# Optimization experiments

Hardware: AMD Instinct MI355X
Metric: run time of the kernel (lower is better)

## Reference

```python
import jax, jax.numpy as jnp
import numpy as np

D_MODEL, N_HEADS = 768, 12
D_K = D_MODEL // N_HEADS
NEG = -1e9


def setup_inputs() -> dict:
    key = jax.random.key(0)
    ks = jax.random.split(key, 12)
    B, S, D = 2, 4096, D_MODEL
    s = 1.0 / np.sqrt(D)
    inp = {
        'query': jax.random.normal(ks[0], (B, S, D), jnp.float32),
        'key': jax.random.normal(ks[1], (B, S, D), jnp.float32),
        'value': jax.random.normal(ks[2], (B, S, D), jnp.float32),
        'mask': jnp.ones((B, S), jnp.int32),
        'Wq': jax.random.normal(ks[3], (D, D), jnp.float32) * s,
        'bq': jnp.zeros((D,), jnp.float32),
        'Wk': jax.random.normal(ks[4], (D, D), jnp.float32) * s,
        'bk': jnp.zeros((D,), jnp.float32),
        'Wv': jax.random.normal(ks[5], (D, D), jnp.float32) * s,
        'bv': jnp.zeros((D,), jnp.float32),
        'Wo': jax.random.normal(ks[6], (D, D), jnp.float32) * s,
        'bo': jnp.zeros((D,), jnp.float32),
    }
    return inp


def reference(query, key, value, mask, Wq, bq, Wk, bk, Wv, bv, Wo, bo):
    B, Sq, D = query.shape
    Sk = key.shape[1]
    # torch Linear: x @ W.T + b; weights stored [out, in]
    def proj(x, W, b, S):
        return (x @ W.T + b).reshape(B, S, N_HEADS, D_K).transpose(0, 2, 1, 3)
    Q = proj(query, Wq, bq, Sq)   # [B,H,Sq,Dk]
    K = proj(key, Wk, bk, Sk)
    V = proj(value, Wv, bv, Sk)
    scores = jnp.einsum('bhqd,bhkd->bhqk', Q, K) / jnp.sqrt(jnp.float32(D_K))
    # padding mask on keys: [B,1,1,Sk]
    scores = jnp.where(mask[:, None, None, :] == 0, NEG, scores)
    # causal mask (triu, diagonal=1)
    causal = jnp.triu(jnp.ones((Sq, Sk), bool), k=1)
    scores = jnp.where(causal[None, None], NEG, scores)
    attn = jax.nn.softmax(scores, axis=-1)
    out = jnp.einsum('bhqk,bhkd->bhqd', attn, V)
    out = out.transpose(0, 2, 1, 3).reshape(B, Sq, D)
    return out @ Wo.T + bo
```

## Files before the change

kernel.cpp:

```cpp
#include <hip/hip_runtime.h>
#include <hip/hip_bf16.h>

#define D_MODEL 768
#define N_HEADS 12
#define D_K     64
#define NEG_INF (-1e9f)
#define SCALE_Q 0.1803368801111154f
#define W_ELEMS (D_MODEL * D_MODEL)
#define PS_PAD  72
#define RED_PAD 36

typedef __attribute__((ext_vector_type(8))) short          bf16x8;
typedef __attribute__((ext_vector_type(4))) float          floatx4;
typedef __attribute__((ext_vector_type(4))) unsigned short ushortx4;
typedef __attribute__((ext_vector_type(2))) unsigned int   uintx2;

static __device__ __forceinline__ unsigned short f2bf(float f) {
    unsigned u = __builtin_bit_cast(unsigned, f);
    u += 0x7FFFu + ((u >> 16) & 1u);
    return (unsigned short)(u >> 16);
}

static __device__ __forceinline__ void gload_lds16(const void* g, void* l) {
    __builtin_amdgcn_global_load_lds(
        (const __attribute__((address_space(1))) void*)g,
        (__attribute__((address_space(3))) void*)l, 16, 0, 0);
}

__global__ __launch_bounds__(256) void convert_w4(
    const float* __restrict__ W0, const float* __restrict__ W1,
    const float* __restrict__ W2, const float* __restrict__ W3,
    unsigned short* __restrict__ out)
{
    const float* src[4] = {W0, W1, W2, W3};
    const float* W = src[blockIdx.y];
    unsigned short* o = out + (size_t)blockIdx.y * W_ELEMS;
    const int i = (blockIdx.x * 256 + threadIdx.x) * 4;
    float4 v = *(const float4*)(W + i);
    ushortx4 h = { f2bf(v.x), f2bf(v.y), f2bf(v.z), f2bf(v.w) };
    *(ushortx4*)(o + i) = h;
}

__global__ __launch_bounds__(256) void convert_a3(
    const float* __restrict__ A0, const float* __restrict__ A1,
    const float* __restrict__ A2,
    unsigned short* __restrict__ O0, unsigned short* __restrict__ O1,
    unsigned short* __restrict__ O2)
{
    const int z = blockIdx.y;
    const float* A = (z == 0) ? A0 : (z == 1) ? A1 : A2;
    unsigned short* O = (z == 0) ? O0 : (z == 1) ? O1 : O2;
    const int i = (blockIdx.x * 256 + threadIdx.x) * 4;
    float4 v = *(const float4*)(A + i);
    ushortx4 h = { f2bf(v.x), f2bf(v.y), f2bf(v.z), f2bf(v.w) };
    *(ushortx4*)(O + i) = h;
}

template <bool QKV>
__global__ __launch_bounds__(256) void gemm128(
    const unsigned short* __restrict__ A0, const unsigned short* __restrict__ A1,
    const unsigned short* __restrict__ A2,
    const unsigned short* __restrict__ W0, const unsigned short* __restrict__ W1,
    const unsigned short* __restrict__ W2,
    const float* __restrict__ b0, const float* __restrict__ b1,
    const float* __restrict__ b2,
    void* __restrict__ C0, void* __restrict__ C1, void* __restrict__ C2,
    int S)
{
    __shared__ __align__(16) unsigned short As[128 * 32];
    __shared__ __align__(16) unsigned short Bs[128 * 32];

    const int z = QKV ? blockIdx.z : 0;
    const unsigned short* A = (z == 0) ? A0 : (z == 1) ? A1 : A2;
    const unsigned short* W = (z == 0) ? W0 : (z == 1) ? W1 : W2;
    const float* bias       = (z == 0) ? b0 : (z == 1) ? b1 : b2;
    void* C                 = (z == 0) ? C0 : (z == 1) ? C1 : C2;
    const float scale = (QKV && z == 0) ? SCALE_Q : 1.0f;
    const int mode = QKV ? ((z == 2) ? 3 : 1) : 0;

    const int tid  = threadIdx.x;
    const int wave = tid >> 6;
    const int lane = tid & 63;
    const int quad = lane >> 4;
    const int l16  = lane & 15;
    const int m0 = blockIdx.x * 128;
    const int n0 = blockIdx.y * 128;
    const int wm = (wave & 1) * 64;
    const int wn = (wave >> 1) * 64;
    const int sr = lane >> 2;
    const int sc = (lane & 3) << 3;

    const floatx4 zero4 = {0.f, 0.f, 0.f, 0.f};
    floatx4 acc[4][4];
    #pragma unroll
    for (int i = 0; i < 4; ++i)
        #pragma unroll
        for (int j = 0; j < 4; ++j) acc[i][j] = zero4;

    for (int k0 = 0; k0 < D_MODEL; k0 += 32) {
        #pragma unroll
        for (int c = 0; c < 2; ++c) {
            const int row = wave * 32 + c * 16;
            gload_lds16(A + (size_t)(m0 + row + sr) * D_MODEL + k0 + sc,
                        As + row * 32);
            gload_lds16(W + (size_t)(n0 + row + sr) * D_MODEL + k0 + sc,
                        Bs + row * 32);
        }
        __syncthreads();

        bf16x8 af[4], bfr[4];
        #pragma unroll
        for (int i = 0; i < 4; ++i)
            af[i] = *(const bf16x8*)(As + (wm + i * 16 + l16) * 32 + quad * 8);
        #pragma unroll
        for (int j = 0; j < 4; ++j)
            bfr[j] = *(const bf16x8*)(Bs + (wn + j * 16 + l16) * 32 + quad * 8);
        #pragma unroll
        for (int i = 0; i < 4; ++i)
            #pragma unroll
            for (int j = 0; j < 4; ++j)
                acc[i][j] = __builtin_amdgcn_mfma_f32_16x16x32_bf16(
                    bfr[j], af[i], acc[i][j], 0, 0, 0);
        __syncthreads();
    }

    #pragma unroll
    for (int i = 0; i < 4; ++i) {
        const int m = m0 + wm + i * 16 + l16;
        #pragma unroll
        for (int j = 0; j < 4; ++j) {
            const int nb = n0 + wn + j * 16 + quad * 4;
            const float4 bv = *(const float4*)(bias + nb);
            float v0 = (acc[i][j][0] + bv.x) * scale;
            float v1 = (acc[i][j][1] + bv.y) * scale;
            float v2 = (acc[i][j][2] + bv.z) * scale;
            float v3 = (acc[i][j][3] + bv.w) * scale;
            if (mode == 0) {
                float4 o = {v0, v1, v2, v3};
                *(float4*)((float*)C + (size_t)m * D_MODEL + nb) = o;
            } else if (mode == 1) {
                ushortx4 o = {f2bf(v0), f2bf(v1), f2bf(v2), f2bf(v3)};
                *(ushortx4*)((unsigned short*)C + (size_t)m * D_MODEL + nb) = o;
            } else {
                const int bb = m / S, s = m - bb * S;
                const int hh = nb >> 6, d = nb & 63;
                unsigned short* base = (unsigned short*)C +
                    ((size_t)(bb * N_HEADS + hh) * D_K + d) * S + s;
                base[0]             = f2bf(v0);
                base[(size_t)S]     = f2bf(v1);
                base[(size_t)S * 2] = f2bf(v2);
                base[(size_t)S * 3] = f2bf(v3);
            }
        }
    }
}

union FlashSmem {
    struct {
        unsigned short KsF[16 * 512];
        unsigned short VtsF[16 * 512];
    } kv;
    struct {
        float red[2][64 * RED_PAD];
        float redl[2][32];
    } ep;
};

__global__ __launch_bounds__(256, 3) void flash_attn(
    const unsigned short* __restrict__ Qp,
    const unsigned short* __restrict__ Kp,
    const unsigned short* __restrict__ VpT,
    const int* __restrict__ mask,
    unsigned short* __restrict__ O,
    int S)
{
    __shared__ __align__(16) FlashSmem sm;
    __shared__ __align__(16) unsigned short Ps[4][32 * PS_PAD];
    __shared__ __align__(16) float mskf[128];

    const int L  = blockIdx.x;
    const int bh = L % 24;
    const int p  = L / 24;
    const int h  = bh % 12;
    const int b  = bh / 12;
    const int nqt = S >> 6;
    const int tid  = threadIdx.x;
    const int wave = tid >> 6;
    const int qw   = wave & 1;
    const int kw   = wave >> 1;
    const int lane = tid & 63;
    const int quad = lane >> 4;
    const int l16  = lane & 15;
    const int ksl  = kw * 64;

    const unsigned short* Kbase = Kp  + (size_t)(b * S) * D_MODEL + h * D_K;
    const unsigned short* Vbase = VpT + (size_t)(b * N_HEADS + h) * D_K * S;
    unsigned short* Psw = Ps[wave];

    const floatx4 zero4 = {0.f, 0.f, 0.f, 0.f};
    const short one_bf = (short)0x3F80;
    const bf16x8 ones = {one_bf, one_bf, one_bf, one_bf,
                         one_bf, one_bf, one_bf, one_bf};

    #pragma unroll
    for (int sel = 0; sel < 2; ++sel) {
        const int qt = sel ? (nqt - 1 - p) : p;
        const int q0 = qt * 64;
        const int qs = q0 + qw * 32;

        bf16x8 qf[2][2];
        #pragma unroll
        for (int qg = 0; qg < 2; ++qg) {
            const size_t rowQ = (size_t)(b * S + qs + qg * 16 + l16) * D_MODEL + h * D_K;
            qf[qg][0] = *(const bf16x8*)(Qp + rowQ + quad * 8);
            qf[qg][1] = *(const bf16x8*)(Qp + rowQ + 32 + quad * 8);
        }

        floatx4 accO[2][4];
        floatx4 accL[2];
        #pragma unroll
        for (int qg = 0; qg < 2; ++qg) {
            accL[qg] = zero4;
            #pragma unroll
            for (int dt = 0; dt < 4; ++dt) accO[qg][dt] = zero4;
        }

        const int ni = (qt >> 1) + 1;
        for (int kt = 0; kt < ni; ++kt) {
            const int k0 = kt * 128;
            #pragma unroll
            for (int c = 0; c < 4; ++c) {
                const int kg = wave * 2 + (c >> 1);
                const int kh = c & 1;
                gload_lds16(Kbase + (size_t)(k0 + kg * 16 + l16) * D_MODEL + kh * 32 + quad * 8,
                            sm.kv.KsF + (kg * 2 + kh) * 512);
                const int dt = wave;
                const int kq = c;
                gload_lds16(Vbase + (size_t)(dt * 16 + l16) * S + k0 + kq * 32 + quad * 8,
                            sm.kv.VtsF + (dt * 4 + kq) * 512);
            }
            if (tid < 128)
                mskf[tid] = (mask[b * S + k0 + tid] == 0) ? NEG_INF : 0.f;
            __syncthreads();

            const int kb = k0 + ksl;
            if (kb <= q0 + 63) {
                const bool diag = (kb + 63 > qs);

                #pragma unroll
                for (int nt = 0; nt < 4; ++nt) {
                    const floatx4 minit = *(const floatx4*)(mskf + ksl + nt * 16 + quad * 4);
                    const int kgf = (kw * 4 + nt) * 2;
                    const bf16x8 kf0 = *(const bf16x8*)(sm.kv.KsF + kgf * 512 + lane * 8);
                    const bf16x8 kf1 = *(const bf16x8*)(sm.kv.KsF + (kgf + 1) * 512 + lane * 8);
                    #pragma unroll
                    for (int qg = 0; qg < 2; ++qg) {
                        floatx4 c = minit;
                        c = __builtin_amdgcn_mfma_f32_16x16x32_bf16(kf0, qf[qg][0], c, 0, 0, 0);
                        c = __builtin_amdgcn_mfma_f32_16x16x32_bf16(kf1, qf[qg][1], c, 0, 0, 0);
                        if (diag) {
                            const int kk = kb + nt * 16 + quad * 4;
                            const int qq = qs + qg * 16 + l16;
                            #pragma unroll
                            for (int r = 0; r < 4; ++r)
                                if (kk + r > qq) c[r] = NEG_INF;
                        }
                        const float e0 = __builtin_exp2f(c[0]);
                        const float e1 = __builtin_exp2f(c[1]);
                        const float e2 = __builtin_exp2f(c[2]);
                        const float e3 = __builtin_exp2f(c[3]);
                        uintx2 pk;
                        pk[0] = __builtin_amdgcn_perm(__builtin_bit_cast(unsigned, e1),
                                                      __builtin_bit_cast(unsigned, e0), 0x07060302u);
                        pk[1] = __builtin_amdgcn_perm(__builtin_bit_cast(unsigned, e3),
                                                      __builtin_bit_cast(unsigned, e2), 0x07060302u);
                        *(uintx2*)(Psw + (qg * 16 + l16) * PS_PAD + nt * 16 + quad * 4) = pk;
                    }
                }

                #pragma unroll
                for (int kh = 0; kh < 2; ++kh) {
                    bf16x8 pf[2];
                    #pragma unroll
                    for (int qg = 0; qg < 2; ++qg)
                        pf[qg] = *(const bf16x8*)(Psw + (qg * 16 + l16) * PS_PAD + kh * 32 + quad * 8);
                    #pragma unroll
                    for (int dt = 0; dt < 4; ++dt) {
                        const bf16x8 vf = *(const bf16x8*)(
                            sm.kv.VtsF + (dt * 4 + kw * 2 + kh) * 512 + lane * 8);
                        #pragma unroll
                        for (int qg = 0; qg < 2; ++qg)
                            accO[qg][dt] = __builtin_amdgcn_mfma_f32_16x16x32_bf16(
                                pf[qg], vf, accO[qg][dt], 0, 0, 0);
                    }
                    #pragma unroll
                    for (int qg = 0; qg < 2; ++qg)
                        accL[qg] = __builtin_amdgcn_mfma_f32_16x16x32_bf16(
                            pf[qg], ones, accL[qg], 0, 0, 0);
                }
            }
            __syncthreads();
        }

        if (kw == 1) {
            float* rb = sm.ep.red[qw];
            #pragma unroll
            for (int qg = 0; qg < 2; ++qg) {
                #pragma unroll
                for (int dt = 0; dt < 4; ++dt)
                    *(floatx4*)(rb + (dt * 16 + l16) * RED_PAD + qg * 16 + quad * 4) = accO[qg][dt];
                if (l16 == 0)
                    *(floatx4*)(sm.ep.redl[qw] + qg * 16 + quad * 4) = accL[qg];
            }
        }
        __syncthreads();
        if (kw == 0) {
            const float* rb = sm.ep.red[qw];
            #pragma unroll
            for (int qg = 0; qg < 2; ++qg) {
                accL[qg] += *(const floatx4*)(sm.ep.redl[qw] + qg * 16 + quad * 4);
                #pragma unroll
                for (int dt = 0; dt < 4; ++dt)
                    accO[qg][dt] += *(const floatx4*)(rb + (dt * 16 + l16) * RED_PAD + qg * 16 + quad * 4);
                #pragma unroll
                for (int r = 0; r < 4; ++r) {
                    const float inv = 1.f / accL[qg][r];
                    const int gq = qs + qg * 16 + quad * 4 + r;
                    unsigned short* ob = O + (size_t)(b * S + gq) * D_MODEL + h * D_K;
                    #pragma unroll
                    for (int dt = 0; dt < 4; ++dt)
                        ob[dt * 16 + l16] = f2bf(accO[qg][dt][r] * inv);
                }
            }
        }
        __syncthreads();
    }
}

extern "C" void kernel_launch(void* const* d_in, const int* in_sizes, int n_in,
                              void* d_out, int out_size, void* d_ws, size_t ws_size,
                              hipStream_t stream) {
    const float* query = (const float*)d_in[0];
    const float* key   = (const float*)d_in[1];
    const float* value = (const float*)d_in[2];
    const int*   mask  = (const int*)d_in[3];
    const float* Wq = (const float*)d_in[4];
    const float* bq = (const float*)d_in[5];
    const float* Wk = (const float*)d_in[6];
    const float* bk = (const float*)d_in[7];
    const float* Wv = (const float*)d_in[8];
    const float* bv = (const float*)d_in[9];
    const float* Wo = (const float*)d_in[10];
    const float* bo = (const float*)d_in[11];

    const int B  = 2;
    const int BS = in_sizes[3];
    const int S  = BS / B;
    const int M  = BS;

    unsigned short* Qp  = (unsigned short*)d_ws;
    unsigned short* Kp  = Qp  + (size_t)M * D_MODEL;
    unsigned short* VpT = Kp  + (size_t)M * D_MODEL;
    unsigned short* Obf = VpT + (size_t)M * D_MODEL;
    unsigned short* Wbf = Obf + (size_t)M * D_MODEL;
    unsigned short* Wqb = Wbf;
    unsigned short* Wkb = Wbf + (size_t)W_ELEMS;
    unsigned short* Wvb = Wbf + (size_t)W_ELEMS * 2;
    unsigned short* Wob = Wbf + (size_t)W_ELEMS * 3;
    unsigned short* ka = (unsigned short*)d_out;
    unsigned short* va = ka + (size_t)M * D_MODEL;

    dim3 blk(256);
    convert_w4<<<dim3(W_ELEMS / 1024, 4), blk, 0, stream>>>(Wq, Wk, Wv, Wo, Wbf);
    convert_a3<<<dim3((M * D_MODEL) / 1024, 3), blk, 0, stream>>>(
        query, key, value, Obf, ka, va);

    gemm128<true><<<dim3(M / 128, D_MODEL / 128, 3), blk, 0, stream>>>(
        Obf, ka, va, Wqb, Wkb, Wvb, bq, bk, bv, Qp, Kp, VpT, S);

    flash_attn<<<768, blk, 0, stream>>>(Qp, Kp, VpT, mask, Obf, S);

    gemm128<false><<<dim3(M / 128, D_MODEL / 128, 1), blk, 0, stream>>>(
        Obf, Obf, Obf, Wob, Wob, Wob, bo, bo, bo,
        d_out, d_out, d_out, S);
}
```

Before: 320.8 us.

## Shrink attention tiles to one query tile per block and retile output GEMM

The attention kernel changes from paired query tiles per block (768 blocks, 128-key steps) to one 64-query tile per block (1536 blocks), launched heaviest-first, with 64-key steps and the P buffer moved into the shared-memory union. It skips the fully masked diagonal sub-block and raises the occupancy target to 5 blocks per CU. The output projection now uses a templated GEMM with 64-row tiles, doubling its block count. The aim is better load balance and occupancy in exchange for more loop iterations, more barriers, and less K/V reuse per block.

New measurement: 352.3 us. 1.1x slower.

```diff
diff --git a/kernel.cpp b/kernel.cpp
--- a/kernel.cpp
+++ b/kernel.cpp
@@ -7,7 +7,7 @@
 #define NEG_INF (-1e9f)
 #define SCALE_Q 0.1803368801111154f
 #define W_ELEMS (D_MODEL * D_MODEL)
-#define PS_PAD  72
+#define PS_PAD  40
 #define RED_PAD 36
 
 typedef __attribute__((ext_vector_type(8))) short          bf16x8;
@@ -56,8 +56,8 @@
     *(ushortx4*)(O + i) = h;
 }
 
-template <bool QKV>
-__global__ __launch_bounds__(256) void gemm128(
+template <int TM, bool QKV>
+__global__ __launch_bounds__(256) void gemm_bt(
     const unsigned short* __restrict__ A0, const unsigned short* __restrict__ A1,
     const unsigned short* __restrict__ A2,
     const unsigned short* __restrict__ W0, const unsigned short* __restrict__ W1,
@@ -67,7 +67,8 @@
     void* __restrict__ C0, void* __restrict__ C1, void* __restrict__ C2,
     int S)
 {
-    __shared__ __align__(16) unsigned short As[128 * 32];
+    constexpr int NI = TM / 32;
+    __shared__ __align__(16) unsigned short As[TM * 32];
     __shared__ __align__(16) unsigned short Bs[128 * 32];
 
     const int z = QKV ? blockIdx.z : 0;
@@ -83,40 +84,44 @@
     const int lane = tid & 63;
     const int quad = lane >> 4;
     const int l16  = lane & 15;
-    const int m0 = blockIdx.x * 128;
+    const int m0 = blockIdx.x * TM;
     const int n0 = blockIdx.y * 128;
-    const int wm = (wave & 1) * 64;
+    const int wm = (wave & 1) * (TM / 2);
     const int wn = (wave >> 1) * 64;
     const int sr = lane >> 2;
     const int sc = (lane & 3) << 3;
 
     const floatx4 zero4 = {0.f, 0.f, 0.f, 0.f};
-    floatx4 acc[4][4];
+    floatx4 acc[NI][4];
     #pragma unroll
-    for (int i = 0; i < 4; ++i)
+    for (int i = 0; i < NI; ++i)
         #pragma unroll
         for (int j = 0; j < 4; ++j) acc[i][j] = zero4;
 
     for (int k0 = 0; k0 < D_MODEL; k0 += 32) {
+        #pragma unroll
+        for (int c = 0; c < TM / 64; ++c) {
+            const int row = wave * (TM / 4) + c * 16;
+            gload_lds16(A + (size_t)(m0 + row + sr) * D_MODEL + k0 + sc,
+                        As + row * 32);
+        }
         #pragma unroll
         for (int c = 0; c < 2; ++c) {
             const int row = wave * 32 + c * 16;
-            gload_lds16(A + (size_t)(m0 + row + sr) * D_MODEL + k0 + sc,
-                        As + row * 32);
             gload_lds16(W + (size_t)(n0 + row + sr) * D_MODEL + k0 + sc,
                         Bs + row * 32);
         }
         __syncthreads();
 
-        bf16x8 af[4], bfr[4];
-        #pragma unroll
-        for (int i = 0; i < 4; ++i)
+        bf16x8 af[NI], bfr[4];
+        #pragma unroll
+        for (int i = 0; i < NI; ++i)
             af[i] = *(const bf16x8*)(As + (wm + i * 16 + l16) * 32 + quad * 8);
         #pragma unroll
         for (int j = 0; j < 4; ++j)
             bfr[j] = *(const bf16x8*)(Bs + (wn + j * 16 + l16) * 32 + quad * 8);
         #pragma unroll
-        for (int i = 0; i < 4; ++i)
+        for (int i = 0; i < NI; ++i)
             #pragma unroll
             for (int j = 0; j < 4; ++j)
                 acc[i][j] = __builtin_amdgcn_mfma_f32_16x16x32_bf16(
@@ -125,7 +130,7 @@
     }
 
     #pragma unroll
-    for (int i = 0; i < 4; ++i) {
+    for (int i = 0; i < NI; ++i) {
         const int m = m0 + wm + i * 16 + l16;
         #pragma unroll
         for (int j = 0; j < 4; ++j) {
@@ -157,8 +162,9 @@
 
 union FlashSmem {
     struct {
-        unsigned short KsF[16 * 512];
-        unsigned short VtsF[16 * 512];
+        unsigned short KsF[8 * 512];
+        unsigned short VtsF[8 * 512];
+        unsigned short Ps[4][32 * PS_PAD];
     } kv;
     struct {
         float red[2][64 * RED_PAD];
@@ -166,7 +172,7 @@
     } ep;
 };
 
-__global__ __launch_bounds__(256, 3) void flash_attn(
+__global__ __launch_bounds__(256, 5) void flash_attn(
     const unsigned short* __restrict__ Qp,
     const unsigned short* __restrict__ Kp,
     const unsigned short* __restrict__ VpT,
@@ -175,15 +181,14 @@
     int S)
 {
     __shared__ __align__(16) FlashSmem sm;
-    __shared__ __align__(16) unsigned short Ps[4][32 * PS_PAD];
-    __shared__ __align__(16) float mskf[128];
+    __shared__ __align__(16) float mskf[64];
 
     const int L  = blockIdx.x;
     const int bh = L % 24;
-    const int p  = L / 24;
+    const int nqt = S >> 6;
+    const int qt = (nqt - 1) - (L / 24);
     const int h  = bh % 12;
     const int b  = bh / 12;
-    const int nqt = S >> 6;
     const int tid  = threadIdx.x;
     const int wave = tid >> 6;
     const int qw   = wave & 1;
@@ -191,149 +196,134 @@
     const int lane = tid & 63;
     const int quad = lane >> 4;
     const int l16  = lane & 15;
-    const int ksl  = kw * 64;
+
+    const int q0 = qt * 64;
+    const int qs = q0 + qw * 32;
 
     const unsigned short* Kbase = Kp  + (size_t)(b * S) * D_MODEL + h * D_K;
     const unsigned short* Vbase = VpT + (size_t)(b * N_HEADS + h) * D_K * S;
-    unsigned short* Psw = Ps[wave];
 
     const floatx4 zero4 = {0.f, 0.f, 0.f, 0.f};
     const short one_bf = (short)0x3F80;
     const bf16x8 ones = {one_bf, one_bf, one_bf, one_bf,
                          one_bf, one_bf, one_bf, one_bf};
 
+    bf16x8 qf[2][2];
     #pragma unroll
-    for (int sel = 0; sel < 2; ++sel) {
-        const int qt = sel ? (nqt - 1 - p) : p;
-        const int q0 = qt * 64;
-        const int qs = q0 + qw * 32;
-
-        bf16x8 qf[2][2];
-        #pragma unroll
-        for (int qg = 0; qg < 2; ++qg) {
-            const size_t rowQ = (size_t)(b * S + qs + qg * 16 + l16) * D_MODEL + h * D_K;
-            qf[qg][0] = *(const bf16x8*)(Qp + rowQ + quad * 8);
-            qf[qg][1] = *(const bf16x8*)(Qp + rowQ + 32 + quad * 8);
-        }
-
-        floatx4 accO[2][4];
-        floatx4 accL[2];
-        #pragma unroll
-        for (int qg = 0; qg < 2; ++qg) {
-            accL[qg] = zero4;
-            #pragma unroll
-            for (int dt = 0; dt < 4; ++dt) accO[qg][dt] = zero4;
-        }
-
-        const int ni = (qt >> 1) + 1;
-        for (int kt = 0; kt < ni; ++kt) {
-            const int k0 = kt * 128;
-            #pragma unroll
-            for (int c = 0; c < 4; ++c) {
-                const int kg = wave * 2 + (c >> 1);
-                const int kh = c & 1;
-                gload_lds16(Kbase + (size_t)(k0 + kg * 16 + l16) * D_MODEL + kh * 32 + quad * 8,
-                            sm.kv.KsF + (kg * 2 + kh) * 512);
-                const int dt = wave;
-                const int kq = c;
-                gload_lds16(Vbase + (size_t)(dt * 16 + l16) * S + k0 + kq * 32 + quad * 8,
-                            sm.kv.VtsF + (dt * 4 + kq) * 512);
-            }
-            if (tid < 128)
-                mskf[tid] = (mask[b * S + k0 + tid] == 0) ? NEG_INF : 0.f;
-            __syncthreads();
-
-            const int kb = k0 + ksl;
-            if (kb <= q0 + 63) {
-                const bool diag = (kb + 63 > qs);
-
+    for (int qg = 0; qg < 2; ++qg) {
+        const size_t rowQ = (size_t)(b * S + qs + qg * 16 + l16) * D_MODEL + h * D_K;
+        qf[qg][0] = *(const bf16x8*)(Qp + rowQ + quad * 8);
+        qf[qg][1] = *(const bf16x8*)(Qp + rowQ + 32 + quad * 8);
+    }
+
+    floatx4 accO[2][4];
+    floatx4 accL[2];
+    #pragma unroll
+    for (int qg = 0; qg < 2; ++qg) {
+        accL[qg] = zero4;
+        #pragma unroll
+        for (int dt = 0; dt < 4; ++dt) accO[qg][dt] = zero4;
+    }
+
+    unsigned short* Psw = sm.kv.Ps[wave];
+
+    for (int kt = 0; kt <= qt; ++kt) {
+        const int k0 = kt * 64;
+        #pragma unroll
+        for (int c = 0; c < 2; ++c) {
+            gload_lds16(Kbase + (size_t)(k0 + wave * 16 + l16) * D_MODEL + c * 32 + quad * 8,
+                        sm.kv.KsF + (wave * 2 + c) * 512);
+            gload_lds16(Vbase + (size_t)(wave * 16 + l16) * S + k0 + c * 32 + quad * 8,
+                        sm.kv.VtsF + (wave * 2 + c) * 512);
+        }
+        if (tid < 64)
+            mskf[tid] = (mask[b * S + k0 + tid] == 0) ? NEG_INF : 0.f;
+        __syncthreads();
+
+        const bool skip = (kt == qt) && (kw == 1) && (qw == 0);
+        if (!skip) {
+            const bool diag = (kt == qt) && (kw == qw);
+            const int kb = k0 + kw * 32;
+
+            #pragma unroll
+            for (int nt = 0; nt < 2; ++nt) {
+                const floatx4 minit = *(const floatx4*)(mskf + kw * 32 + nt * 16 + quad * 4);
+                const int kgf = (kw * 2 + nt) * 2;
+                const bf16x8 kf0 = *(const bf16x8*)(sm.kv.KsF + kgf * 512 + lane * 8);
+                const bf16x8 kf1 = *(const bf16x8*)(sm.kv.KsF + (kgf + 1) * 512 + lane * 8);
                 #pragma unroll
-                for (int nt = 0; nt < 4; ++nt) {
-                    const floatx4 minit = *(const floatx4*)(mskf + ksl + nt * 16 + quad * 4);
-                    const int kgf = (kw * 4 + nt) * 2;
-                    const bf16x8 kf0 = *(const bf16x8*)(sm.kv.KsF + kgf * 512 + lane * 8);
-                    const bf16x8 kf1 = *(const bf16x8*)(sm.kv.KsF + (kgf + 1) * 512 + lane * 8);
-                    #pragma unroll
-                    for (int qg = 0; qg < 2; ++qg) {
-                        floatx4 c = minit;
-                        c = __builtin_amdgcn_mfma_f32_16x16x32_bf16(kf0, qf[qg][0], c, 0, 0, 0);
-                        c = __builtin_amdgcn_mfma_f32_16x16x32_bf16(kf1, qf[qg][1], c, 0, 0, 0);
-                        if (diag) {
-                            const int kk = kb + nt * 16 + quad * 4;
-                            const int qq = qs + qg * 16 + l16;
-                            #pragma unroll
-                            for (int r = 0; r < 4; ++r)
-                                if (kk + r > qq) c[r] = NEG_INF;
-                        }
-                        const float e0 = __builtin_exp2f(c[0]);
-                        const float e1 = __builtin_exp2f(c[1]);
-                        const float e2 = __builtin_exp2f(c[2]);
-                        const float e3 = __builtin_exp2f(c[3]);
-                        uintx2 pk;
-                        pk[0] = __builtin_amdgcn_perm(__builtin_bit_cast(unsigned, e1),
-                                                      __builtin_bit_cast(unsigned, e0), 0x07060302u);
-                        pk[1] = __builtin_amdgcn_perm(__builtin_bit_cast(unsigned, e3),
-                                                      __builtin_bit_cast(unsigned, e2), 0x07060302u);
-                        *(uintx2*)(Psw + (qg * 16 + l16) * PS_PAD + nt * 16 + quad * 4) = pk;
+                for (int qg = 0; qg < 2; ++qg) {
+                    floatx4 c = minit;
+                    c = __builtin_amdgcn_mfma_f32_16x16x32_bf16(kf0, qf[qg][0], c, 0, 0, 0);
+                    c = __builtin_amdgcn_mfma_f32_16x16x32_bf16(kf1, qf[qg][1], c, 0, 0, 0);
+                    if (diag) {
+                        const int kk = kb + nt * 16 + quad * 4;
+                        const int qq = qs + qg * 16 + l16;
+                        #pragma unroll
+                        for (int r = 0; r < 4; ++r)
+                            if (kk + r > qq) c[r] = NEG_INF;
                     }
-                }
-
-                #pragma unroll
-                for (int kh = 0; kh < 2; ++kh) {
-                    bf16x8 pf[2];
-                    #pragma unroll
-                    for (int qg = 0; qg < 2; ++qg)
-                        pf[qg] = *(const bf16x8*)(Psw + (qg * 16 + l16) * PS_PAD + kh * 32 + quad * 8);
-                    #pragma unroll
-                    for (int dt = 0; dt < 4; ++dt) {
-                        const bf16x8 vf = *(const bf16x8*)(
-                            sm.kv.VtsF + (dt * 4 + kw * 2 + kh) * 512 + lane * 8);
-                        #pragma unroll
-                        for (int qg = 0; qg < 2; ++qg)
-                            accO[qg][dt] = __builtin_amdgcn_mfma_f32_16x16x32_bf16(
-                                pf[qg], vf, accO[qg][dt], 0, 0, 0);
-                    }
-                    #pragma unroll
-                    for (int qg = 0; qg < 2; ++qg)
-                        accL[qg] = __builtin_amdgcn_mfma_f32_16x16x32_bf16(
-                            pf[qg], ones, accL[qg], 0, 0, 0);
+                    const float e0 = __builtin_exp2f(c[0]);
+                    const float e1 = __builtin_exp2f(c[1]);
+                    const float e2 = __builtin_exp2f(c[2]);
+                    const float e3 = __builtin_exp2f(c[3]);
+                    uintx2 pk;
+                    pk[0] = __builtin_amdgcn_perm(__builtin_bit_cast(unsigned, e1),
+                                                  __builtin_bit_cast(unsigned, e0), 0x07060302u);
+                    pk[1] = __builtin_amdgcn_perm(__builtin_bit_cast(unsigned, e3),
+                                                  __builtin_bit_cast(unsigned, e2), 0x07060302u);
+                    *(uintx2*)(Psw + (qg * 16 + l16) * PS_PAD + nt * 16 + quad * 4) = pk;
                 }
             }
-            __syncthreads();
-        }
-
-        if (kw == 1) {
-            float* rb = sm.ep.red[qw];
+
+            bf16x8 vf[4];
+            #pragma unroll
+            for (int dt = 0; dt < 4; ++dt)
+                vf[dt] = *(const bf16x8*)(sm.kv.VtsF + (dt * 2 + kw) * 512 + lane * 8);
             #pragma unroll
             for (int qg = 0; qg < 2; ++qg) {
+                const bf16x8 pf = *(const bf16x8*)(Psw + (qg * 16 + l16) * PS_PAD + quad * 8);
                 #pragma unroll
                 for (int dt = 0; dt < 4; ++dt)
-                    *(floatx4*)(rb + (dt * 16 + l16) * RED_PAD + qg * 16 + quad * 4) = accO[qg][dt];
-                if (l16 == 0)
-                    *(floatx4*)(sm.ep.redl[qw] + qg * 16 + quad * 4) = accL[qg];
+                    accO[qg][dt] = __builtin_amdgcn_mfma_f32_16x16x32_bf16(
+                        pf, vf[dt], accO[qg][dt], 0, 0, 0);
+                accL[qg] = __builtin_amdgcn_mfma_f32_16x16x32_bf16(
+                    pf, ones, accL[qg], 0, 0, 0);
             }
         }
         __syncthreads();
-        if (kw == 0) {
-            const float* rb = sm.ep.red[qw];
-            #pragma unroll
-            for (int qg = 0; qg < 2; ++qg) {
-                accL[qg] += *(const floatx4*)(sm.ep.redl[qw] + qg * 16 + quad * 4);
+    }
+
+    if (kw == 1) {
+        float* rb = sm.ep.red[qw];
+        #pragma unroll
+        for (int qg = 0; qg < 2; ++qg) {
+            #pragma unroll
+            for (int dt = 0; dt < 4; ++dt)
+                *(floatx4*)(rb + (dt * 16 + l16) * RED_PAD + qg * 16 + quad * 4) = accO[qg][dt];
+            if (l16 == 0)
+                *(floatx4*)(sm.ep.redl[qw] + qg * 16 + quad * 4) = accL[qg];
+        }
+    }
+    __syncthreads();
+    if (kw == 0) {
+        const float* rb = sm.ep.red[qw];
+        #pragma unroll
+        for (int qg = 0; qg < 2; ++qg) {
+            accL[qg] += *(const floatx4*)(sm.ep.redl[qw] + qg * 16 + quad * 4);
+            #pragma unroll
+            for (int dt = 0; dt < 4; ++dt)
+                accO[qg][dt] += *(const floatx4*)(rb + (dt * 16 + l16) * RED_PAD + qg * 16 + quad * 4);
+            #pragma unroll
+            for (int r = 0; r < 4; ++r) {
+                const float inv = 1.f / accL[qg][r];
+                const int gq = qs + qg * 16 + quad * 4 + r;
+                unsigned short* ob = O + (size_t)(b * S + gq) * D_MODEL + h * D_K;
                 #pragma unroll
                 for (int dt = 0; dt < 4; ++dt)
-                    accO[qg][dt] += *(const floatx4*)(rb + (dt * 16 + l16) * RED_PAD + qg * 16 + quad * 4);
-                #pragma unroll
-                for (int r = 0; r < 4; ++r) {
-                    const float inv = 1.f / accL[qg][r];
-                    const int gq = qs + qg * 16 + quad * 4 + r;
-                    unsigned short* ob = O + (size_t)(b * S + gq) * D_MODEL + h * D_K;
-                    #pragma unroll
-                    for (int dt = 0; dt < 4; ++dt)
-                        ob[dt * 16 + l16] = f2bf(accO[qg][dt][r] * inv);
-                }
+                    ob[dt * 16 + l16] = f2bf(accO[qg][dt][r] * inv);
             }
         }
-        __syncthreads();
     }
 }
 
@@ -375,12 +365,12 @@
     convert_a3<<<dim3((M * D_MODEL) / 1024, 3), blk, 0, stream>>>(
         query, key, value, Obf, ka, va);
 
-    gemm128<true><<<dim3(M / 128, D_MODEL / 128, 3), blk, 0, stream>>>(
+    gemm_bt<128, true><<<dim3(M / 128, D_MODEL / 128, 3), blk, 0, stream>>>(
         Obf, ka, va, Wqb, Wkb, Wvb, bq, bk, bv, Qp, Kp, VpT, S);
 
-    flash_attn<<<768, blk, 0, stream>>>(Qp, Kp, VpT, mask, Obf, S);
-
-    gemm128<false><<<dim3(M / 128, D_MODEL / 128, 1), blk, 0, stream>>>(
+    flash_attn<<<24 * (S / 64), blk, 0, stream>>>(Qp, Kp, VpT, mask, Obf, S);
+
+    gemm_bt<64, false><<<dim3(M / 64, D_MODEL / 128, 1), blk, 0, stream>>>(
         Obf, Obf, Obf, Wob, Wob, Wob, bo, bo, bo,
         d_out, d_out, d_out, S);
 }
```
